# Kernel optimization log

Measured on AMD Instinct MI355X. Metric: run time of the kernel, lower is better.

## Reference

```python
import jax, jax.numpy as jnp
import numpy as np

B, L, H, E = 4, 1024, 8, 64


def setup_inputs() -> dict:
    key = jax.random.key(0)
    kq, kk, kv = jax.random.split(key, 3)
    queries = jax.random.normal(kq, (B, L, H, E), dtype=jnp.float32)
    keys = jax.random.normal(kk, (B, L, H, E), dtype=jnp.float32)
    values = jax.random.normal(kv, (B, L, H, E), dtype=jnp.float32)
    attn_mask = jnp.zeros((1,), dtype=bool)  # unused by the module
    return {"queries": queries, "keys": keys, "values": values, "attn_mask": attn_mask}


def _spectral_interaction(queries, keys, values):
    # queries/keys/values: [B, L, H, E] (L == S here, so the torch truncation is a no-op)
    b, l, h, e = queries.shape
    qh = jnp.transpose(queries, (0, 2, 1, 3))  # [B,H,L,E]
    kh = jnp.transpose(keys[:, :l], (0, 2, 1, 3))  # [B,H,L,E]
    # cosine-similarity score matrix, exponentiated: exp(q.k / (|q||k|))
    q_norm = jnp.linalg.norm(qh, axis=-1, keepdims=True)  # [B,H,L,1]
    k_norm = jnp.linalg.norm(kh, axis=-1, keepdims=True)  # [B,H,L,1]
    dot_num = jnp.einsum('bhle,bhse->bhls', qh, kh)        # [B,H,L,L]
    dot_den = q_norm * jnp.swapaxes(k_norm, -1, -2)        # [B,H,L,L] via broadcast
    sim = jnp.exp(dot_num / dot_den)                       # [B,H,L,L]

    # FFT-domain double softmax over frequency bins
    inter_fft = jnp.fft.rfft(sim, axis=-1).real            # [B,H,L,F], F=L//2+1
    scale = 1.0 / np.sqrt(e)
    A = jax.nn.softmax(
        jnp.sum(jax.nn.softmax(scale * inter_fft, axis=-1), axis=-2),
        axis=-1,
    )                                                      # [B,H,F]  (dropout = identity in eval)
    A = A[:, :, None, :]                                   # [B,H,1,F]

    # gate the real part of the value spectrum, keep imag part, reconstruct
    vh = jnp.transpose(values[:, :l], (0, 2, 3, 1))        # [B,H,E,L]
    v_fft = jnp.fft.rfft(vh, axis=-1)                      # [B,H,E,F] complex
    Vc = jax.lax.complex(A * v_fft.real, v_fft.imag)       # [B,H,E,F]
    V = jnp.fft.irfft(Vc, n=l, axis=-1)                    # [B,H,E,L]
    return jnp.transpose(V, (0, 3, 2, 1))                  # [B,L,E,H] (matches torch permute(0,3,2,1))


def reference(queries, keys, values, attn_mask):
    # attn_mask is unused by the original forward
    return _spectral_interaction(queries, keys, values)
```

## Files before the change

### kernel.cpp

```cpp
#include <hip/hip_runtime.h>
#include <hip/hip_bf16.h>
#include <math.h>

#define B_ 4
#define L_ 1024
#define H_ 8
#define E_ 64
#define N_ 1024
#define NF_ 513
#define SCALE_ 0.125f
#define HE_ (H_ * E_)
#define ZP_ 1104

typedef _Float16 f16x8 __attribute__((ext_vector_type(8)));
typedef float f32x4 __attribute__((ext_vector_type(4)));

__device__ __forceinline__ int dr4(int x) {
    const int r = (int)(__brev((unsigned)x) >> 22);
    return ((r & 0x155) << 1) | ((r >> 1) & 0x155);
}

__device__ __forceinline__ int PD(int i) { return i + (i >> 4) + (i >> 6); }

__device__ __forceinline__ float2 cmulw(float2 v, float2 w, float dir) {
    const float wi = dir * w.y;
    return make_float2(v.x * w.x - v.y * wi, v.x * wi + v.y * w.x);
}

__device__ __forceinline__ void r4c(const float2 x0, const float2 x1,
                                    const float2 x2, const float2 x3,
                                    const float dir,
                                    float2& y0, float2& y1, float2& y2, float2& y3) {
    const float ax = x0.x + x2.x, ay = x0.y + x2.y;
    const float bx = x0.x - x2.x, by = x0.y - x2.y;
    const float cx = x1.x + x3.x, cy = x1.y + x3.y;
    const float dx = x1.x - x3.x, dy = x1.y - x3.y;
    y0 = make_float2(ax + cx, ay + cy);
    y2 = make_float2(ax - cx, ay - cy);
    y1 = make_float2(bx - dir * dy, by + dir * dx);
    y3 = make_float2(bx + dir * dy, by - dir * dx);
}

__device__ __forceinline__ void fill_tw(float2* tw, int t) {
    for (int i = t; i < 1024; i += 256) {
        float sv, cv;
        sincosf(6.283185307179586f * (float)i / 1024.0f, &sv, &cv);
        tw[PD(i)] = make_float2(cv, sv);
    }
}

__device__ __forceinline__ void wfft_dit4(float2* z, const float2* tw, int lane, float dir) {
    #pragma unroll
    for (int st = 0; st < 5; ++st) {
        const int l2q = 2 * st, qs = 1 << l2q;
        const int step = 1 << (8 - l2q);
        #pragma unroll
        for (int ib = 0; ib < 4; ++ib) {
            const int j = (st == 0) ? (((lane & 15) << 2) | (lane >> 4)) + 64 * ib
                                    : lane + 64 * ib;
            const int pos = j & (qs - 1);
            const int base = ((j >> l2q) << (l2q + 2)) + pos;
            const int i0 = PD(base), i1 = PD(base + qs), i2 = PD(base + 2 * qs), i3 = PD(base + 3 * qs);
            float2 x0 = z[i0], x1 = z[i1], x2 = z[i2], x3 = z[i3];
            if (st) {
                x1 = cmulw(x1, tw[PD(pos * step)], dir);
                x2 = cmulw(x2, tw[PD(2 * pos * step)], dir);
                x3 = cmulw(x3, tw[PD(3 * pos * step)], dir);
            }
            float2 y0, y1, y2, y3;
            r4c(x0, x1, x2, x3, dir, y0, y1, y2, y3);
            z[i0] = y0; z[i1] = y1; z[i2] = y2; z[i3] = y3;
        }
        __builtin_amdgcn_wave_barrier();
    }
}

__device__ __forceinline__ void wfft_dif4(float2* z, const float2* tw, int lane, float dir) {
    #pragma unroll
    for (int st = 4; st >= 0; --st) {
        const int l2q = 2 * st, qs = 1 << l2q;
        const int step = 1 << (8 - l2q);
        #pragma unroll
        for (int ib = 0; ib < 4; ++ib) {
            const int j = (st == 0) ? (((lane & 15) << 2) | (lane >> 4)) + 64 * ib
                                    : lane + 64 * ib;
            const int pos = j & (qs - 1);
            const int base = ((j >> l2q) << (l2q + 2)) + pos;
            const int i0 = PD(base), i1 = PD(base + qs), i2 = PD(base + 2 * qs), i3 = PD(base + 3 * qs);
            const float2 x0 = z[i0], x1 = z[i1], x2 = z[i2], x3 = z[i3];
            float2 s0, s1, s2, s3;
            r4c(x0, x1, x2, x3, dir, s0, s1, s2, s3);
            if (st) {
                s1 = cmulw(s1, tw[PD(pos * step)], dir);
                s2 = cmulw(s2, tw[PD(2 * pos * step)], dir);
                s3 = cmulw(s3, tw[PD(3 * pos * step)], dir);
            }
            z[i0] = s0; z[i1] = s1; z[i2] = s2; z[i3] = s3;
        }
        __builtin_amdgcn_wave_barrier();
    }
}

__global__ __launch_bounds__(256) void k_prep(const float* __restrict__ K,
                                              _Float16* __restrict__ Kh) {
    const int i = blockIdx.x * 256 + threadIdx.x;
    if (i >= B_ * L_ * H_) return;
    const float* p = K + (size_t)i * E_;
    float ss = 0.0f;
    #pragma unroll
    for (int j = 0; j < 16; ++j) {
        const float4 v = *(const float4*)(p + j * 4);
        ss += v.x * v.x + v.y * v.y + v.z * v.z + v.w * v.w;
    }
    const float r = rsqrtf(ss);
    _Float16* out = Kh + (size_t)i * E_;
    #pragma unroll
    for (int e = 0; e < E_; e += 8) {
        const float4 x = *(const float4*)(p + e);
        const float4 y = *(const float4*)(p + e + 4);
        f16x8 o;
        o[0] = (_Float16)(x.x * r); o[1] = (_Float16)(x.y * r);
        o[2] = (_Float16)(x.z * r); o[3] = (_Float16)(x.w * r);
        o[4] = (_Float16)(y.x * r); o[5] = (_Float16)(y.y * r);
        o[6] = (_Float16)(y.z * r); o[7] = (_Float16)(y.w * r);
        *(f16x8*)(out + e) = o;
    }
}

__global__ __attribute__((amdgpu_flat_work_group_size(256, 256), amdgpu_waves_per_eu(2, 3)))
void k_qkfft(const float* __restrict__ Q,
             const _Float16* __restrict__ Kh,
             float* __restrict__ G) {
    __shared__ float2 s_z[4 * ZP_];
    __shared__ float2 s_tw[ZP_];
    __shared__ float s_acc[NF_];
    __shared__ float s_red[32];

    const int t = threadIdx.x;
    const int bid = blockIdx.x;
    const int bh = bid >> 6;
    const int chunk = bid & 63;
    const int b = bh >> 3, h = bh & 7;
    const int l0 = chunk * 16;

    const int c = t & 15;
    const int g = (t >> 4) & 3;
    const int w = t >> 6;
    const int lane = t & 63, wid = w;

    fill_tw(s_tw, t);
    for (int kk = t; kk < NF_; kk += 256) s_acc[kk] = 0.0f;

    const float* qrow = Q + (((size_t)b * L_ + l0 + c) * H_ + h) * E_;
    const float4 x0 = *(const float4*)(qrow + g * 8);
    const float4 y0 = *(const float4*)(qrow + g * 8 + 4);
    const float4 x1 = *(const float4*)(qrow + 32 + g * 8);
    const float4 y1 = *(const float4*)(qrow + 32 + g * 8 + 4);
    float ss = x0.x * x0.x + x0.y * x0.y + x0.z * x0.z + x0.w * x0.w
             + y0.x * y0.x + y0.y * y0.y + y0.z * y0.z + y0.w * y0.w
             + x1.x * x1.x + x1.y * x1.y + x1.z * x1.z + x1.w * x1.w
             + y1.x * y1.x + y1.y * y1.y + y1.z * y1.z + y1.w * y1.w;
    ss += __shfl_xor(ss, 16);
    ss += __shfl_xor(ss, 32);
    const float qn = rsqrtf(ss);
    f16x8 af0, af1;
    af0[0] = (_Float16)(x0.x * qn); af0[1] = (_Float16)(x0.y * qn);
    af0[2] = (_Float16)(x0.z * qn); af0[3] = (_Float16)(x0.w * qn);
    af0[4] = (_Float16)(y0.x * qn); af0[5] = (_Float16)(y0.y * qn);
    af0[6] = (_Float16)(y0.z * qn); af0[7] = (_Float16)(y0.w * qn);
    af1[0] = (_Float16)(x1.x * qn); af1[1] = (_Float16)(x1.y * qn);
    af1[2] = (_Float16)(x1.z * qn); af1[3] = (_Float16)(x1.w * qn);
    af1[4] = (_Float16)(y1.x * qn); af1[5] = (_Float16)(y1.y * qn);
    af1[6] = (_Float16)(y1.z * qn); af1[7] = (_Float16)(y1.w * qn);

    f32x4 acc[16];
    #pragma unroll
    for (int n = 0; n < 16; ++n) acc[n] = (f32x4){0.0f, 0.0f, 0.0f, 0.0f};

    #pragma unroll
    for (int n = 0; n < 16; ++n) {
        const int j = w * 256 + n * 16 + c;
        const int s = dr4(j);
        const f16x8* bp = (const f16x8*)(Kh + (((size_t)b * L_ + s) * H_ + h) * E_);
        const f16x8 b0 = bp[g];
        const f16x8 b1 = bp[4 + g];
        acc[n] = __builtin_amdgcn_mfma_f32_16x16x32_f16(af0, b0, acc[n], 0, 0, 0);
        acc[n] = __builtin_amdgcn_mfma_f32_16x16x32_f16(af1, b1, acc[n], 0, 0, 0);
        if ((n & 3) == 3) __builtin_amdgcn_sched_barrier(0);
    }

    #pragma unroll
    for (int n = 0; n < 16; ++n) {
        #pragma unroll
        for (int r = 0; r < 4; ++r) acc[n][r] = __expf(acc[n][r]);
    }

    const float dir = -1.0f;

    #pragma unroll
    for (int rr = 0; rr < 2; ++rr) {
        __syncthreads();
        {
            const int gq = g - 2 * rr;
            if (gq == 0 || gq == 1) {
                float2* z01 = s_z + (2 * gq) * ZP_;
                #pragma unroll
                for (int n = 0; n < 16; ++n) {
                    const int ps = PD(w * 256 + n * 16 + c);
                    z01[ps]       = make_float2(acc[n][0], acc[n][1]);
                    z01[ZP_ + ps] = make_float2(acc[n][2], acc[n][3]);
                }
            }
        }
        __syncthreads();

        #pragma unroll
        for (int st = 0; st < 5; ++st) {
            const int l2q = 2 * st, qs = 1 << l2q;
            const int j = (st == 0) ? (((t & 63) << 2) | (t >> 6)) : t;
            const int pos = j & (qs - 1);
            const int base = ((j >> l2q) << (l2q + 2)) + pos;
            const int i0 = PD(base), i1 = PD(base + qs), i2 = PD(base + 2 * qs), i3 = PD(base + 3 * qs);
            float2 w1, w2, w3;
            if (st) {
                const int step = 1 << (8 - l2q);
                w1 = s_tw[PD(pos * step)];
                w2 = s_tw[PD(2 * pos * step)];
                w3 = s_tw[PD(3 * pos * step)];
            }
            #pragma unroll
            for (int q = 0; q < 4; ++q) {
                float2* z = s_z + q * ZP_;
                float2 a0 = z[i0], a1 = z[i1], a2 = z[i2], a3 = z[i3];
                if (st) { a1 = cmulw(a1, w1, dir); a2 = cmulw(a2, w2, dir); a3 = cmulw(a3, w3, dir); }
                float2 b0, b1, b2, b3;
                r4c(a0, a1, a2, a3, dir, b0, b1, b2, b3);
                z[i0] = b0; z[i1] = b1; z[i2] = b2; z[i3] = b3;
            }
            __syncthreads();
        }

        const int iT = PD(t), iTn = PD((N_ - t) & (N_ - 1));
        const int iU = PD(t + 256), iUn = PD(768 - t);
        float p[8][2], pm[8], sm[8];
        #pragma unroll
        for (int q = 0; q < 4; ++q) {
            const float2* z = s_z + q * ZP_;
            const float2 X0 = z[iT], X0n = z[iTn], X1 = z[iU], X1n = z[iUn];
            const float2 DC = z[0];
            const float2 XN = z[PD(512)];
            const float mA = SCALE_ * DC.x, mB = SCALE_ * DC.y;
            p[2 * q][0]     = __expf(SCALE_ * 0.5f * (X0.x + X0n.x) - mA);
            p[2 * q][1]     = __expf(SCALE_ * 0.5f * (X1.x + X1n.x) - mA);
            p[2 * q + 1][0] = __expf(SCALE_ * 0.5f * (X0.y + X0n.y) - mB);
            p[2 * q + 1][1] = __expf(SCALE_ * 0.5f * (X1.y + X1n.y) - mB);
            pm[2 * q]     = __expf(SCALE_ * XN.x - mA);
            pm[2 * q + 1] = __expf(SCALE_ * XN.y - mB);
            sm[2 * q]     = p[2 * q][0] + p[2 * q][1] + ((t == 0) ? pm[2 * q] : 0.0f);
            sm[2 * q + 1] = p[2 * q + 1][0] + p[2 * q + 1][1] + ((t == 0) ? pm[2 * q + 1] : 0.0f);
        }
        #pragma unroll
        for (int off = 32; off > 0; off >>= 1) {
            #pragma unroll
            for (int q2 = 0; q2 < 8; ++q2) sm[q2] += __shfl_xor(sm[q2], off);
        }
        if (lane == 0) {
            #pragma unroll
            for (int q2 = 0; q2 < 8; ++q2) s_red[4 * q2 + wid] = sm[q2];
        }
        __syncthreads();
        float add0 = 0.0f, add1 = 0.0f, addm = 0.0f;
        #pragma unroll
        for (int q2 = 0; q2 < 8; ++q2) {
            const float inv = 1.0f / (s_red[4 * q2] + s_red[4 * q2 + 1] +
                                      s_red[4 * q2 + 2] + s_red[4 * q2 + 3]);
            add0 += p[q2][0] * inv;
            add1 += p[q2][1] * inv;
            addm += pm[q2] * inv;
        }
        s_acc[t]       += add0;
        s_acc[t + 256] += add1;
        if (t == 0) s_acc[512] += addm;
    }
    __syncthreads();

    float* Gp = G + (size_t)bh * NF_;
    for (int kk = t; kk < NF_; kk += 256) atomicAdd(&Gp[kk], s_acc[kk]);
}

__global__ __launch_bounds__(256) void k_vfft(const float* __restrict__ V,
                                              const float* __restrict__ G,
                                              float* __restrict__ Out) {
    __shared__ float2 s_zv[4 * ZP_];
    __shared__ float2 s_tw[ZP_];
    __shared__ float s_A[NF_];
    __shared__ float s_red[8];

    const int t = threadIdx.x;
    const int bid = blockIdx.x;
    const int bh = bid >> 3, pg = bid & 7;
    const int b = bh >> 3, h = bh & 7;
    const int w = t >> 6, lane = t & 63;
    const int e0 = 2 * (pg * 4 + w);

    fill_tw(s_tw, t);

    {
        const float* Gp = G + (size_t)bh * NF_;
        const float g0 = Gp[t];
        const float g1 = Gp[t + 256];
        const float g2 = (t == 0) ? Gp[512] : -1e30f;
        float m = fmaxf(fmaxf(g0, g1), g2);
        #pragma unroll
        for (int off = 32; off > 0; off >>= 1) m = fmaxf(m, __shfl_xor(m, off));
        if (lane == 0) s_red[w] = m;
        __syncthreads();
        m = fmaxf(fmaxf(s_red[0], s_red[1]), fmaxf(s_red[2], s_red[3]));
        const float p0 = __expf(g0 - m), p1 = __expf(g1 - m);
        const float p2 = (t == 0) ? __expf(g2 - m) : 0.0f;
        float s = p0 + p1 + p2;
        #pragma unroll
        for (int off = 32; off > 0; off >>= 1) s += __shfl_xor(s, off);
        __syncthreads();
        if (lane == 0) s_red[4 + w] = s;
        __syncthreads();
        s = s_red[4] + s_red[5] + s_red[6] + s_red[7];
        const float inv = 1.0f / s;
        s_A[t] = p0 * inv;
        s_A[t + 256] = p1 * inv;
        if (t == 0) s_A[512] = p2 * inv;
    }
    __syncthreads();

    float2* z = s_zv + w * ZP_;

    #pragma unroll
    for (int jb = 0; jb < 16; ++jb) {
        const int s = lane + 64 * jb;
        const float* vp = V + (((size_t)b * L_ + s) * H_ + h) * E_ + e0;
        z[PD(dr4(s))] = make_float2(vp[0], vp[1]);
    }
    __builtin_amdgcn_wave_barrier();

    wfft_dit4(z, s_tw, lane, -1.0f);

    #pragma unroll
    for (int ib = 0; ib < 8; ++ib) {
        const int k = lane + 64 * ib;
        const int kp = (N_ - k) & (N_ - 1);
        const int ik = PD(k), ikp = PD(kp);
        const float2 X1 = z[ik];
        const float2 X2 = z[ikp];
        const float reV1 = 0.5f * (X1.x + X2.x);
        const float imV1 = 0.5f * (X1.y - X2.y);
        const float reV2 = 0.5f * (X1.y + X2.y);
        const float imV2 = 0.5f * (X2.x - X1.x);
        const float a = s_A[k];
        z[ik] = make_float2(a * reV1 - imV2, imV1 + a * reV2);
        if (kp != k)
            z[ikp] = make_float2(a * reV1 + imV2, -imV1 + a * reV2);
    }
    if (lane == 0) {
        const float2 X = z[PD(512)];
        const float a = s_A[512];
        z[PD(512)] = make_float2(a * X.x, a * X.y);
    }
    __builtin_amdgcn_wave_barrier();

    wfft_dif4(z, s_tw, lane, +1.0f);

    const float invN = 1.0f / (float)N_;
    #pragma unroll
    for (int jb = 0; jb < 16; ++jb) {
        const int p = lane + 64 * jb;
        const int l = dr4(p);
        const float2 r = z[PD(p)];
        const size_t o = (((size_t)b * L_ + l) * E_ + e0) * H_ + h;
        Out[o] = r.x * invN;
        Out[o + H_] = r.y * invN;
    }
}

extern "C" void kernel_launch(void* const* d_in, const int* in_sizes, int n_in,
                              void* d_out, int out_size, void* d_ws, size_t ws_size,
                              hipStream_t stream) {
    const float* Q = (const float*)d_in[0];
    const float* K = (const float*)d_in[1];
    const float* V = (const float*)d_in[2];
    float* out = (float*)d_out;

    float* ws = (float*)d_ws;
    float* G     = ws;
    _Float16* Kh = (_Float16*)(ws + B_ * H_ * NF_);

    hipMemsetAsync(G, 0, (size_t)B_ * H_ * NF_ * sizeof(float), stream);
    k_prep<<<(B_ * L_ * H_ + 255) / 256, 256, 0, stream>>>(K, Kh);
    k_qkfft<<<B_ * H_ * (L_ / 16), 256, 0, stream>>>(Q, Kh, G);
    k_vfft<<<B_ * H_ * (E_ / 8), 256, 0, stream>>>(V, G, out);
}
```

Baseline: 117.8 us.

## Keep QK FFT twiddles in registers and use wave-local barriers for early stages

In the score-FFT kernel, the shared twiddle table becomes per-thread twiddles in registers, computed once with sincos and complex squaring. The first four radix-4 stages are wave-local, so they use wave barriers instead of block-wide syncs, and only the final cross-wave stage needs __syncthreads. The shared accumulator is replaced by register accumulators that are atomically added straight to global memory. The waves-per-EU hint is also raised. The digit-reversal input ordering in the wave FFT helpers is dropped, which relies on the load ordering elsewhere matching.

Measured after the change: 122.7 us. +4.2%, slower.

```diff
diff --git a/kernel.cpp b/kernel.cpp
--- a/kernel.cpp
+++ b/kernel.cpp
@@ -21,6 +21,10 @@
 }
 
 __device__ __forceinline__ int PD(int i) { return i + (i >> 4) + (i >> 6); }
+
+__device__ __forceinline__ float2 cmul(float2 a, float2 b) {
+    return make_float2(a.x * b.x - a.y * b.y, a.x * b.y + a.y * b.x);
+}
 
 __device__ __forceinline__ float2 cmulw(float2 v, float2 w, float dir) {
     const float wi = dir * w.y;
@@ -56,8 +60,7 @@
         const int step = 1 << (8 - l2q);
         #pragma unroll
         for (int ib = 0; ib < 4; ++ib) {
-            const int j = (st == 0) ? (((lane & 15) << 2) | (lane >> 4)) + 64 * ib
-                                    : lane + 64 * ib;
+            const int j = lane + 64 * ib;
             const int pos = j & (qs - 1);
             const int base = ((j >> l2q) << (l2q + 2)) + pos;
             const int i0 = PD(base), i1 = PD(base + qs), i2 = PD(base + 2 * qs), i3 = PD(base + 3 * qs);
@@ -82,8 +85,7 @@
         const int step = 1 << (8 - l2q);
         #pragma unroll
         for (int ib = 0; ib < 4; ++ib) {
-            const int j = (st == 0) ? (((lane & 15) << 2) | (lane >> 4)) + 64 * ib
-                                    : lane + 64 * ib;
+            const int j = lane + 64 * ib;
             const int pos = j & (qs - 1);
             const int base = ((j >> l2q) << (l2q + 2)) + pos;
             const int i0 = PD(base), i1 = PD(base + qs), i2 = PD(base + 2 * qs), i3 = PD(base + 3 * qs);
@@ -127,13 +129,11 @@
     }
 }
 
-__global__ __attribute__((amdgpu_flat_work_group_size(256, 256), amdgpu_waves_per_eu(2, 3)))
+__global__ __attribute__((amdgpu_flat_work_group_size(256, 256), amdgpu_waves_per_eu(2, 4)))
 void k_qkfft(const float* __restrict__ Q,
              const _Float16* __restrict__ Kh,
              float* __restrict__ G) {
     __shared__ float2 s_z[4 * ZP_];
-    __shared__ float2 s_tw[ZP_];
-    __shared__ float s_acc[NF_];
     __shared__ float s_red[32];
 
     const int t = threadIdx.x;
@@ -148,8 +148,18 @@
     const int w = t >> 6;
     const int lane = t & 63, wid = w;
 
-    fill_tw(s_tw, t);
-    for (int kk = t; kk < NF_; kk += 256) s_acc[kk] = 0.0f;
+    float2 tw1[4], tw2[4], tw3[4];
+    #pragma unroll
+    for (int st = 1; st <= 4; ++st) {
+        const int qs = 1 << (2 * st);
+        const int pos = t & (qs - 1);
+        const int step = 1 << (8 - 2 * st);
+        float sv, cv;
+        sincosf(6.283185307179586f * (float)(pos * step) / 1024.0f, &sv, &cv);
+        const float2 w1 = make_float2(cv, -sv);
+        const float2 w2 = cmul(w1, w1);
+        tw1[st - 1] = w1; tw2[st - 1] = w2; tw3[st - 1] = cmul(w2, w1);
+    }
 
     const float* qrow = Q + (((size_t)b * L_ + l0 + c) * H_ + h) * E_;
     const float4 x0 = *(const float4*)(qrow + g * 8);
@@ -196,10 +206,10 @@
     }
 
     const float dir = -1.0f;
+    float racc0 = 0.0f, racc1 = 0.0f, raccN = 0.0f;
 
     #pragma unroll
     for (int rr = 0; rr < 2; ++rr) {
-        __syncthreads();
         {
             const int gq = g - 2 * rr;
             if (gq == 0 || gq == 1) {
@@ -212,33 +222,46 @@
                 }
             }
         }
-        __syncthreads();
-
-        #pragma unroll
-        for (int st = 0; st < 5; ++st) {
+        __builtin_amdgcn_wave_barrier();
+
+        #pragma unroll
+        for (int st = 0; st < 4; ++st) {
             const int l2q = 2 * st, qs = 1 << l2q;
-            const int j = (st == 0) ? (((t & 63) << 2) | (t >> 6)) : t;
-            const int pos = j & (qs - 1);
-            const int base = ((j >> l2q) << (l2q + 2)) + pos;
+            const int pos = t & (qs - 1);
+            const int base = ((t >> l2q) << (l2q + 2)) + pos;
             const int i0 = PD(base), i1 = PD(base + qs), i2 = PD(base + 2 * qs), i3 = PD(base + 3 * qs);
-            float2 w1, w2, w3;
-            if (st) {
-                const int step = 1 << (8 - l2q);
-                w1 = s_tw[PD(pos * step)];
-                w2 = s_tw[PD(2 * pos * step)];
-                w3 = s_tw[PD(3 * pos * step)];
-            }
             #pragma unroll
             for (int q = 0; q < 4; ++q) {
                 float2* z = s_z + q * ZP_;
                 float2 a0 = z[i0], a1 = z[i1], a2 = z[i2], a3 = z[i3];
-                if (st) { a1 = cmulw(a1, w1, dir); a2 = cmulw(a2, w2, dir); a3 = cmulw(a3, w3, dir); }
+                if (st) {
+                    a1 = cmul(a1, tw1[st - 1]);
+                    a2 = cmul(a2, tw2[st - 1]);
+                    a3 = cmul(a3, tw3[st - 1]);
+                }
                 float2 b0, b1, b2, b3;
                 r4c(a0, a1, a2, a3, dir, b0, b1, b2, b3);
                 z[i0] = b0; z[i1] = b1; z[i2] = b2; z[i3] = b3;
             }
-            __syncthreads();
-        }
+            __builtin_amdgcn_wave_barrier();
+        }
+        __syncthreads();
+
+        {
+            const int i0 = PD(t), i1 = PD(t + 256), i2 = PD(t + 512), i3 = PD(t + 768);
+            #pragma unroll
+            for (int q = 0; q < 4; ++q) {
+                float2* z = s_z + q * ZP_;
+                float2 a0 = z[i0];
+                float2 a1 = cmul(z[i1], tw1[3]);
+                float2 a2 = cmul(z[i2], tw2[3]);
+                float2 a3 = cmul(z[i3], tw3[3]);
+                float2 b0, b1, b2, b3;
+                r4c(a0, a1, a2, a3, dir, b0, b1, b2, b3);
+                z[i0] = b0; z[i1] = b1; z[i2] = b2; z[i3] = b3;
+            }
+        }
+        __syncthreads();
 
         const int iT = PD(t), iTn = PD((N_ - t) & (N_ - 1));
         const int iU = PD(t + 256), iUn = PD(768 - t);
@@ -269,23 +292,20 @@
             for (int q2 = 0; q2 < 8; ++q2) s_red[4 * q2 + wid] = sm[q2];
         }
         __syncthreads();
-        float add0 = 0.0f, add1 = 0.0f, addm = 0.0f;
         #pragma unroll
         for (int q2 = 0; q2 < 8; ++q2) {
             const float inv = 1.0f / (s_red[4 * q2] + s_red[4 * q2 + 1] +
                                       s_red[4 * q2 + 2] + s_red[4 * q2 + 3]);
-            add0 += p[q2][0] * inv;
-            add1 += p[q2][1] * inv;
-            addm += pm[q2] * inv;
-        }
-        s_acc[t]       += add0;
-        s_acc[t + 256] += add1;
-        if (t == 0) s_acc[512] += addm;
-    }
-    __syncthreads();
+            racc0 += p[q2][0] * inv;
+            racc1 += p[q2][1] * inv;
+            raccN += pm[q2] * inv;
+        }
+    }
 
     float* Gp = G + (size_t)bh * NF_;
-    for (int kk = t; kk < NF_; kk += 256) atomicAdd(&Gp[kk], s_acc[kk]);
+    atomicAdd(&Gp[t], racc0);
+    atomicAdd(&Gp[t + 256], racc1);
+    if (t == 0) atomicAdd(&Gp[512], raccN);
 }
 
 __global__ __launch_bounds__(256) void k_vfft(const float* __restrict__ V,
```
